# Performance work log

Hardware: AMD Instinct MI355X
Metric: run time of the kernel (lower is better)

Reference implementation:

```python
import jax, jax.numpy as jnp
import numpy as np

B, S, DIN, DOUT = 8, 2048, 4096, 11008


def setup_inputs() -> dict:
    key = jax.random.key(0)
    k1, k2, k3 = jax.random.split(key, 3)
    x = jax.random.normal(k1, (B, S, DIN), dtype=jnp.float32)
    # int8 quantized weight in [-128, 127]
    weight_int8 = jax.random.randint(k2, (DOUT, DIN), -128, 128, dtype=jnp.int8)
    # positive per-output-row scales
    weight_scale = jax.random.uniform(k3, (DOUT,), dtype=jnp.float32, minval=1e-4, maxval=1e-2)
    return {"x": x, "weight_int8": weight_int8, "weight_scale": weight_scale}


def reference(x, weight_int8, weight_scale):
    # dequantize: [DOUT, DIN] fp32 weight
    w_fp = weight_int8.astype(jnp.float32) * weight_scale[:, None]
    # F.linear: x @ w.T  -> [B, S, DOUT]
    return jnp.einsum('bsd,od->bso', x, w_fp)
```

## Files before the change

### kernel.cpp

```cpp
#include <hip/hip_runtime.h>
#include <cstdint>
#include <cstddef>

typedef __attribute__((ext_vector_type(4))) int int32x4;
typedef __attribute__((ext_vector_type(16))) int int32x16;

#define DEVI __device__ __forceinline__

constexpr int M = 16384;
constexpr int N = 11008;
constexpr int K = 4096;
constexpr int BM = 256, BN = 256, BK = 64;
constexpr int NT_M = M / BM;
constexpr int NT_N = N / BN;
constexpr int NTILES = K / BK;
constexpr int NWG = NT_M * NT_N;
constexpr int TILE_BYTES = BM * BK;

DEVI void gload_lds16(const void* gsrc, void* ldst) {
  __builtin_amdgcn_global_load_lds(
      (const __attribute__((address_space(1))) unsigned int*)gsrc,
      (__attribute__((address_space(3))) unsigned int*)ldst,
      16, 0, 0);
}

__global__ __launch_bounds__(256) void pack_w_kernel(const int* __restrict__ w32,
                                                     signed char* __restrict__ w8) {
  const int idx = blockIdx.x * 256 + threadIdx.x;
  const int total4 = N * K / 4;
  if (idx < total4) {
    const int4 v = ((const int4*)w32)[idx];
    ((int*)w8)[idx] = (v.x & 255) | ((v.y & 255) << 8) |
                      ((v.z & 255) << 16) | ((v.w & 255) << 24);
  }
}

__global__ __launch_bounds__(256) void quant_x_kernel(const float* __restrict__ x,
                                                      signed char* __restrict__ xq,
                                                      float* __restrict__ sx) {
  const int row = blockIdx.x;
  const int t = threadIdx.x;
  const float4* xr = (const float4*)(x + (size_t)row * K);
  float4 v[4];
  float amax = 0.f;
  #pragma unroll
  for (int c = 0; c < 4; ++c) {
    v[c] = xr[c * 256 + t];
    amax = fmaxf(amax, fmaxf(fmaxf(fabsf(v[c].x), fabsf(v[c].y)),
                             fmaxf(fabsf(v[c].z), fabsf(v[c].w))));
  }
  __shared__ float red[256];
  red[t] = amax;
  __syncthreads();
  #pragma unroll
  for (int s = 128; s >= 1; s >>= 1) {
    if (t < s) red[t] = fmaxf(red[t], red[t + s]);
    __syncthreads();
  }
  const float am = fmaxf(red[0], 1e-20f);
  const float inv = 127.f / am;
  if (t == 0) sx[row] = am * (1.f / 127.f);
  int* xq32 = (int*)(xq + (size_t)row * K);
  #pragma unroll
  for (int c = 0; c < 4; ++c) {
    int q0 = min(127, max(-127, __float2int_rn(v[c].x * inv)));
    int q1 = min(127, max(-127, __float2int_rn(v[c].y * inv)));
    int q2 = min(127, max(-127, __float2int_rn(v[c].z * inv)));
    int q3 = min(127, max(-127, __float2int_rn(v[c].w * inv)));
    xq32[c * 256 + t] = (q0 & 255) | ((q1 & 255) << 8) |
                        ((q2 & 255) << 16) | ((q3 & 255) << 24);
  }
}

__global__ __launch_bounds__(512, 2) void gemm_i8_kernel(const signed char* __restrict__ aq,
                                                         const signed char* __restrict__ wq,
                                                         const float* __restrict__ sx,
                                                         const float* __restrict__ sw,
                                                         float* __restrict__ out) {
  extern __shared__ signed char smem[];
  signed char* lsA = smem;
  signed char* lsB = smem + 4 * TILE_BYTES;

  const int t = threadIdx.x;
  const int w = t >> 6;
  const int l = t & 63;

  const int bid = blockIdx.x;
  const int wg = (bid & 7) * (NWG / 8) + (bid >> 3);
  const int mt = wg / NT_N;
  const int nt = wg % NT_N;
  const int m0 = mt * BM, n0 = nt * BN;

  const bool stA = (w < 4);
  const signed char* src[4];
  int loff[4];
  #pragma unroll
  for (int c = 0; c < 4; ++c) {
    const int q = (w & 3) * 4 + c;
    const int row = (q & 3) * 64 + l;
    const int s = q >> 2;
    const signed char* base = stA ? (aq + (size_t)(m0 + row) * K)
                                  : (wq + (size_t)(n0 + row) * K);
    src[c] = base + s * 16;
    loff[c] = q * 1024;
  }

#define STAGE(tile)                                                           \
  {                                                                           \
    signed char* lbase = (stA ? lsA : lsB) + ((tile) & 3) * TILE_BYTES;       \
    const int koff = (tile) * BK;                                             \
    gload_lds16(src[0] + koff, lbase + loff[0]);                              \
    gload_lds16(src[1] + koff, lbase + loff[1]);                              \
    gload_lds16(src[2] + koff, lbase + loff[2]);                              \
    gload_lds16(src[3] + koff, lbase + loff[3]);                              \
  }

  const int wm = w >> 2, wn = w & 3;
  const int lk = l >> 5;
  const int lr = l & 31;
  int aOff[4], bOff[2];
  #pragma unroll
  for (int i = 0; i < 4; ++i)
    aOff[i] = lk * 4096 + (wm * 128 + i * 32 + lr) * 16;
  #pragma unroll
  for (int j = 0; j < 2; ++j)
    bOff[j] = lk * 4096 + (wn * 64 + j * 32 + lr) * 16;

  int32x16 acc[4][2] = {};
  int32x4 af0[4], bf0[2], af1[4], bf1[2];

#define DSL(tile, sub, AF, BF)                                                \
  {                                                                           \
    const signed char* pA = lsA + ((tile) & 3) * TILE_BYTES + (sub) * 8192;   \
    const signed char* pB = lsB + ((tile) & 3) * TILE_BYTES + (sub) * 8192;   \
    AF[0] = *(const int32x4*)(pA + aOff[0]);                                  \
    AF[1] = *(const int32x4*)(pA + aOff[1]);                                  \
    AF[2] = *(const int32x4*)(pA + aOff[2]);                                  \
    AF[3] = *(const int32x4*)(pA + aOff[3]);                                  \
    BF[0] = *(const int32x4*)(pB + bOff[0]);                                  \
    BF[1] = *(const int32x4*)(pB + bOff[1]);                                  \
  }

#define MFMA8(AF, BF)                                                         \
  __builtin_amdgcn_s_setprio(1);                                              \
  {                                                                           \
    _Pragma("unroll")                                                         \
    for (int i = 0; i < 4; ++i) {                                             \
      acc[i][0] = __builtin_amdgcn_mfma_i32_32x32x32_i8(AF[i], BF[0],         \
                                                        acc[i][0], 0, 0, 0);  \
      acc[i][1] = __builtin_amdgcn_mfma_i32_32x32x32_i8(AF[i], BF[1],         \
                                                        acc[i][1], 0, 0, 0);  \
    }                                                                         \
  }                                                                           \
  __builtin_amdgcn_s_setprio(0);

#define WAITV(n) asm volatile("s_waitcnt vmcnt(" #n ")" ::: "memory");
#define WLGKM(n)                                                              \
  asm volatile("s_waitcnt lgkmcnt(" #n ")" ::: "memory");                     \
  __builtin_amdgcn_sched_barrier(0);
#define BAR() __builtin_amdgcn_s_barrier();

#define ITER(tt)                                                              \
  WAITV(4)                        \
  BAR()                              \
  STAGE(tt + 3)                \
  DSL(tt, 1, af1, bf1)           \
  WLGKM(6)                                            \
  MFMA8(af0, bf0)                                            \
  DSL(tt + 1, 0, af0, bf0)   \
  WLGKM(6)                                            \
  MFMA8(af1, bf1)

  STAGE(0) STAGE(1) STAGE(2)
  WAITV(8)
  BAR()
  DSL(0, 0, af0, bf0)

  #pragma unroll 4
  for (int tb = 0; tb < 60; ++tb) {
    ITER(tb)
  }
  ITER(60)
  WAITV(4) BAR()
  DSL(61, 1, af1, bf1) WLGKM(6) MFMA8(af0, bf0)
  DSL(62, 0, af0, bf0) WLGKM(6) MFMA8(af1, bf1)
  WAITV(0) BAR()
  DSL(62, 1, af1, bf1) WLGKM(6) MFMA8(af0, bf0)
  DSL(63, 0, af0, bf0) WLGKM(6) MFMA8(af1, bf1)
  DSL(63, 1, af1, bf1) WLGKM(6) MFMA8(af0, bf0)
  WLGKM(0) MFMA8(af1, bf1)

  const int rbase = lk * 4;
  float swv[2];
  #pragma unroll
  for (int fj = 0; fj < 2; ++fj) swv[fj] = sw[n0 + wn * 64 + fj * 32 + lr];
  #pragma unroll
  for (int fi = 0; fi < 4; ++fi) {
    #pragma unroll
    for (int r = 0; r < 16; ++r) {
      const int row = (r & 3) + 8 * (r >> 2) + rbase;
      const int grow = m0 + wm * 128 + fi * 32 + row;
      const float sxv = sx[grow];
      float* orow = out + (size_t)grow * N + n0 + wn * 64 + lr;
      #pragma unroll
      for (int fj = 0; fj < 2; ++fj) {
        orow[fj * 32] = (float)acc[fi][fj][r] * sxv * swv[fj];
      }
    }
  }
}

extern "C" void kernel_launch(void* const* d_in, const int* in_sizes, int n_in,
                              void* d_out, int out_size, void* d_ws, size_t ws_size,
                              hipStream_t stream) {
  const float* x = (const float*)d_in[0];
  const int* w32 = (const int*)d_in[1];
  const float* wscale = (const float*)d_in[2];
  float* out = (float*)d_out;

  signed char* xq = (signed char*)d_ws;
  signed char* wq = xq + (size_t)M * K;
  float* sx = (float*)(wq + (size_t)N * K);

  pack_w_kernel<<<(N * K / 4 + 255) / 256, 256, 0, stream>>>(w32, wq);
  quant_x_kernel<<<M, 256, 0, stream>>>(x, xq, sx);
  gemm_i8_kernel<<<NWG, 512, 131072, stream>>>(xq, wq, sx, wscale, out);
}
```

Baseline: 1.033 ms.

## Interleave per-chunk global loads with LDS reads and MFMAs behind barriers

Restructures the K-loop into four sub-phases per tile. Each phase issues one global-to-LDS load chunk, two A fragments and, when needed, B fragments, then runs four MFMAs between workgroup barriers, replacing the earlier double-buffered register-fragment prefetch. The tile mapping also becomes M-fastest (mt = wg&63) instead of N-fastest, which changes L2 reuse. The many added barriers and full lgkmcnt(0) waits remove LDS-read and MFMA overlap within a wave, which risks more stalls.

```diff
diff --git a/kernel.cpp b/kernel.cpp
--- a/kernel.cpp
+++ b/kernel.cpp
@@ -87,8 +87,8 @@
 
   const int bid = blockIdx.x;
   const int wg = (bid & 7) * (NWG / 8) + (bid >> 3);
-  const int mt = wg / NT_N;
-  const int nt = wg % NT_N;
+  const int mt = wg & 63;
+  const int nt = wg >> 6;
   const int m0 = mt * BM, n0 = nt * BN;
 
   const bool stA = (w < 4);
@@ -105,15 +105,12 @@
     loff[c] = q * 1024;
   }
 
-#define STAGE(tile)                                                           \
+#define STG1(tile, c)                                                         \
   {                                                                           \
     signed char* lbase = (stA ? lsA : lsB) + ((tile) & 3) * TILE_BYTES;       \
-    const int koff = (tile) * BK;                                             \
-    gload_lds16(src[0] + koff, lbase + loff[0]);                              \
-    gload_lds16(src[1] + koff, lbase + loff[1]);                              \
-    gload_lds16(src[2] + koff, lbase + loff[2]);                              \
-    gload_lds16(src[3] + koff, lbase + loff[3]);                              \
-  }
+    gload_lds16(src[c] + (tile) * BK, lbase + loff[c]);                       \
+  }
+#define STG_FULL(tile) STG1(tile, 0) STG1(tile, 1) STG1(tile, 2) STG1(tile, 3)
 
   const int wm = w >> 2, wn = w & 3;
   const int lk = l >> 5;
@@ -127,68 +124,78 @@
     bOff[j] = lk * 4096 + (wn * 64 + j * 32 + lr) * 16;
 
   int32x16 acc[4][2] = {};
-  int32x4 af0[4], bf0[2], af1[4], bf1[2];
-
-#define DSL(tile, sub, AF, BF)                                                \
+  int32x4 b0[2], b1[2], aA[2], aB[2], aC[2], aD[2];
+
+#define DSA2(tile, ks, ib, R)                                                 \
   {                                                                           \
-    const signed char* pA = lsA + ((tile) & 3) * TILE_BYTES + (sub) * 8192;   \
-    const signed char* pB = lsB + ((tile) & 3) * TILE_BYTES + (sub) * 8192;   \
-    AF[0] = *(const int32x4*)(pA + aOff[0]);                                  \
-    AF[1] = *(const int32x4*)(pA + aOff[1]);                                  \
-    AF[2] = *(const int32x4*)(pA + aOff[2]);                                  \
-    AF[3] = *(const int32x4*)(pA + aOff[3]);                                  \
-    BF[0] = *(const int32x4*)(pB + bOff[0]);                                  \
-    BF[1] = *(const int32x4*)(pB + bOff[1]);                                  \
-  }
-
-#define MFMA8(AF, BF)                                                         \
+    const signed char* pA = lsA + ((tile) & 3) * TILE_BYTES + (ks) * 8192;    \
+    R[0] = *(const int32x4*)(pA + aOff[ib]);                                  \
+    R[1] = *(const int32x4*)(pA + aOff[(ib) + 1]);                            \
+  }
+#define DSB2(tile, ks, R)                                                     \
+  {                                                                           \
+    const signed char* pB = lsB + ((tile) & 3) * TILE_BYTES + (ks) * 8192;    \
+    R[0] = *(const int32x4*)(pB + bOff[0]);                                   \
+    R[1] = *(const int32x4*)(pB + bOff[1]);                                   \
+  }
+
+#define LGKM0()                                          \
+  asm volatile("s_waitcnt lgkmcnt(0)" ::: "memory");     \
+  __builtin_amdgcn_sched_barrier(0);
+
+#define MFMA4(A2, B2, ib)                                                     \
   __builtin_amdgcn_s_setprio(1);                                              \
-  {                                                                           \
-    _Pragma("unroll")                                                         \
-    for (int i = 0; i < 4; ++i) {                                             \
-      acc[i][0] = __builtin_amdgcn_mfma_i32_32x32x32_i8(AF[i], BF[0],         \
-                                                        acc[i][0], 0, 0, 0);  \
-      acc[i][1] = __builtin_amdgcn_mfma_i32_32x32x32_i8(AF[i], BF[1],         \
-                                                        acc[i][1], 0, 0, 0);  \
-    }                                                                         \
-  }                                                                           \
+  acc[ib][0] = __builtin_amdgcn_mfma_i32_32x32x32_i8(A2[0], B2[0],            \
+                                                     acc[ib][0], 0, 0, 0);    \
+  acc[ib][1] = __builtin_amdgcn_mfma_i32_32x32x32_i8(A2[0], B2[1],            \
+                                                     acc[ib][1], 0, 0, 0);    \
+  acc[(ib) + 1][0] = __builtin_amdgcn_mfma_i32_32x32x32_i8(A2[1], B2[0],      \
+                                                     acc[(ib) + 1][0], 0, 0, 0);\
+  acc[(ib) + 1][1] = __builtin_amdgcn_mfma_i32_32x32x32_i8(A2[1], B2[1],      \
+                                                     acc[(ib) + 1][1], 0, 0, 0);\
   __builtin_amdgcn_s_setprio(0);
 
 #define WAITV(n) asm volatile("s_waitcnt vmcnt(" #n ")" ::: "memory");
-#define WLGKM(n)                                                              \
-  asm volatile("s_waitcnt lgkmcnt(" #n ")" ::: "memory");                     \
-  __builtin_amdgcn_sched_barrier(0);
 #define BAR() __builtin_amdgcn_s_barrier();
 
-#define ITER(tt)                                                              \
-  WAITV(4)                        \
-  BAR()                              \
-  STAGE(tt + 3)                \
-  DSL(tt, 1, af1, bf1)           \
-  WLGKM(6)                                            \
-  MFMA8(af0, bf0)                                            \
-  DSL(tt + 1, 0, af0, bf0)   \
-  WLGKM(6)                                            \
-  MFMA8(af1, bf1)
-
-  STAGE(0) STAGE(1) STAGE(2)
+#define ITER(tt, WV)                                                          \
+                                                     \
+  DSB2(tt, 0, b0) DSA2(tt, 0, 0, aA) STG1(tt + 3, 0)                          \
+  BAR() LGKM0() MFMA4(aA, b0, 0) BAR()                                        \
+                                                   \
+  DSA2(tt, 0, 2, aB) STG1(tt + 3, 1)                                          \
+  BAR() LGKM0() MFMA4(aB, b0, 2) BAR()                                        \
+                                                     \
+  DSB2(tt, 1, b1) DSA2(tt, 1, 0, aC) STG1(tt + 3, 2)                          \
+  BAR() LGKM0() MFMA4(aC, b1, 0) BAR()                                        \
+                               \
+  DSA2(tt, 1, 2, aD) STG1(tt + 3, 3)                                          \
+  WV                                                                          \
+  BAR() LGKM0() MFMA4(aD, b1, 2) BAR()
+
+#define ITERN(tt, WV)                                                         \
+  DSB2(tt, 0, b0) DSA2(tt, 0, 0, aA)                                          \
+  BAR() LGKM0() MFMA4(aA, b0, 0) BAR()                                        \
+  DSA2(tt, 0, 2, aB)                                                          \
+  BAR() LGKM0() MFMA4(aB, b0, 2) BAR()                                        \
+  DSB2(tt, 1, b1) DSA2(tt, 1, 0, aC)                                          \
+  BAR() LGKM0() MFMA4(aC, b1, 0) BAR()                                        \
+  DSA2(tt, 1, 2, aD)                                                          \
+  WV                                                                          \
+  BAR() LGKM0() MFMA4(aD, b1, 2) BAR()
+
+  STG_FULL(0) STG_FULL(1) STG_FULL(2)
   WAITV(8)
   BAR()
-  DSL(0, 0, af0, bf0)
 
   #pragma unroll 4
   for (int tb = 0; tb < 60; ++tb) {
-    ITER(tb)
-  }
-  ITER(60)
-  WAITV(4) BAR()
-  DSL(61, 1, af1, bf1) WLGKM(6) MFMA8(af0, bf0)
-  DSL(62, 0, af0, bf0) WLGKM(6) MFMA8(af1, bf1)
-  WAITV(0) BAR()
-  DSL(62, 1, af1, bf1) WLGKM(6) MFMA8(af0, bf0)
-  DSL(63, 0, af0, bf0) WLGKM(6) MFMA8(af1, bf1)
-  DSL(63, 1, af1, bf1) WLGKM(6) MFMA8(af0, bf0)
-  WLGKM(0) MFMA8(af1, bf1)
+    ITER(tb, WAITV(8))
+  }
+  ITER(60, WAITV(8))
+  ITERN(61, WAITV(4))
+  ITERN(62, WAITV(0))
+  ITERN(63, )
 
   const int rbase = lk * 4;
   float swv[2];
```

Result: slower. 1.198 ms (+15.9%).
